# Kernel tuning notes

Measured on AMD Instinct MI355X. Metric: run time of the kernel, lower is better.

Reference implementation:

```python
import jax, jax.numpy as jnp
import numpy as np
from jax import lax

D_MODEL = 1024
D_STATE = 16
D_CONV = 4
EXPAND = 2
D_INNER = EXPAND * D_MODEL  # 2048
DT_RANK = -(-D_MODEL // 16)  # ceil = 64
BATCH = 2
T = 1024


def setup_inputs() -> dict:
    key = jax.random.key(0)
    ks = jax.random.split(key, 9)
    s = 0.02
    x = jax.random.normal(ks[0], (BATCH, T, D_MODEL), dtype=jnp.float32)
    W_in = jax.random.normal(ks[1], (D_MODEL, 2 * D_INNER), dtype=jnp.float32) * s
    conv_w = jax.random.normal(ks[2], (D_INNER, D_CONV), dtype=jnp.float32) * 0.2
    conv_b = jax.random.normal(ks[3], (D_INNER,), dtype=jnp.float32) * 0.02
    W_xproj = jax.random.normal(ks[4], (D_INNER, DT_RANK + 2 * D_STATE), dtype=jnp.float32) * s
    W_dt = jax.random.normal(ks[5], (DT_RANK, D_INNER), dtype=jnp.float32) * s
    b_dt = jax.random.normal(ks[6], (D_INNER,), dtype=jnp.float32) * 0.02
    A_log = jnp.broadcast_to(jnp.log(jnp.arange(1, D_STATE + 1, dtype=jnp.float32)), (D_INNER, D_STATE)).copy()
    D_param = jnp.ones((D_INNER,), dtype=jnp.float32)
    W_out = jax.random.normal(ks[7], (D_INNER, D_MODEL), dtype=jnp.float32) * s
    return {"x": x, "W_in": W_in, "conv_w": conv_w, "conv_b": conv_b,
            "W_xproj": W_xproj, "W_dt": W_dt, "b_dt": b_dt,
            "A_log": A_log, "D_param": D_param, "W_out": W_out}


def _silu(u):
    return u * jax.nn.sigmoid(u)


def _forward(x, W_in, conv_w, conv_b, W_xproj, W_dt, b_dt, A_log, D_param, W_out):
    B, Tlen, _ = x.shape
    # in_proj and split into x-branch and gate z
    xz = x @ W_in                                   # (B,T,2*d_inner)
    x_b, z = jnp.split(xz, 2, axis=-1)              # each (B,T,d_inner)
    # causal depthwise conv1d: y[t] = sum_k w[:,k] * x[t-d_conv+1+k]
    xpad = jnp.pad(x_b, ((0, 0), (D_CONV - 1, 0), (0, 0)))
    xc = conv_b
    for k in range(D_CONV):
        xc = xc + xpad[:, k:k + Tlen, :] * conv_w[:, k]
    xc = _silu(xc)                                  # (B,T,d_inner)
    # SSM parameter projections
    proj = xc @ W_xproj                             # (B,T,dt_rank+2*d_state)
    delta_raw = proj[..., :DT_RANK]
    B_in = proj[..., DT_RANK:DT_RANK + D_STATE]     # (B,T,d_state)
    C_in = proj[..., DT_RANK + D_STATE:]            # (B,T,d_state)
    delta = jax.nn.softplus(delta_raw @ W_dt + b_dt)  # (B,T,d_inner)
    A = -jnp.exp(A_log)                             # (d_inner,d_state)
    A_bar = jnp.exp(delta[..., None] * A)           # (B,T,d_inner,d_state)
    Bx = delta[..., None] * B_in[:, :, None, :] * xc[..., None]  # (B,T,d_inner,d_state)

    def step(h, ins):
        a_t, bx_t, c_t, xc_t = ins
        h = a_t * h + bx_t                          # (B,d_inner,d_state)
        y_t = jnp.einsum('bds,bs->bd', h, c_t) + D_param * xc_t
        return h, y_t

    h0 = jnp.zeros((B, D_INNER, D_STATE), dtype=x.dtype)
    ins = (jnp.swapaxes(A_bar, 0, 1), jnp.swapaxes(Bx, 0, 1),
           jnp.swapaxes(C_in, 0, 1), jnp.swapaxes(xc, 0, 1))
    _, ys = lax.scan(step, h0, ins)                 # ys: (T,B,d_inner)
    y = jnp.swapaxes(ys, 0, 1) * _silu(z)           # gated
    return y @ W_out                                # (B,T,d_model)


def reference(x, W_in, conv_w, conv_b, W_xproj, W_dt, b_dt, A_log, D_param, W_out):
    return _forward(x, W_in, conv_w, conv_b, W_xproj, W_dt, b_dt, A_log, D_param, W_out)
```

## Files before the change

kernel.cpp:

```cpp
#include <hip/hip_runtime.h>
#include <math.h>

#define BATCH   2
#define TLEN    1024
#define DMODEL  1024
#define DINNER  2048
#define DSTATE  16
#define DTRANK  64
#define NPROJ   (DTRANK + 2*DSTATE)
#define CH      32
#define NCH     (TLEN / CH)

typedef __attribute__((ext_vector_type(8))) short short8;
typedef __attribute__((ext_vector_type(4))) float f32x4;

__device__ __forceinline__ float siluf(float u) {
    return u / (1.0f + __expf(-u));
}
__device__ __forceinline__ float softplusf(float x) {
    return (x > 20.0f) ? x : log1pf(__expf(x));
}
__device__ __forceinline__ unsigned short f2bf(float f) {
    union { float f; unsigned u; } v; v.f = f;
    unsigned r = v.u + 0x7FFF + ((v.u >> 16) & 1);
    return (unsigned short)(r >> 16);
}
__device__ __forceinline__ float bf2f(unsigned short u) {
    union { unsigned u; float f; } v; v.u = (unsigned)u << 16;
    return v.f;
}

#define GLOAD_LDS16(g, l) \
  __builtin_amdgcn_global_load_lds( \
     (const __attribute__((address_space(1))) unsigned int*)(g), \
     (__attribute__((address_space(3))) unsigned int*)(l), 16, 0, 0)

template<int NFRAG, int OUTBF, int EPI>
__global__ __launch_bounds__(256)
void gemm_bf16(const unsigned short* __restrict__ A, int lda,
               const unsigned short* __restrict__ BT, int ldb,
               void* __restrict__ Cv, int ldc, int kchunk,
               const float* __restrict__ bias, size_t zstride)
{
    constexpr int BN = NFRAG * 32;
    __shared__ unsigned short As[128 * 32];
    __shared__ unsigned short Bs[BN * 32];

    const int nwg = gridDim.x * gridDim.y;
    int id = blockIdx.y * gridDim.x + blockIdx.x;
    {
        const int q = nwg >> 3, r = nwg & 7, xcd = id & 7, lid = id >> 3;
        id = (xcd < r ? xcd * (q + 1) : r * (q + 1) + (xcd - r) * q) + lid;
    }
    const int bx = id % gridDim.x, by = id / gridDim.x;

    const int tid  = threadIdx.x;
    const int wid  = tid >> 6;
    const int lane = tid & 63;
    const int brow = by * 128;
    const int bcol = bx * BN;
    const int kbeg = blockIdx.z * kchunk;
    const int wr = (wid >> 1) * 64;
    const int wc = (wid & 1) * (NFRAG * 16);
    const int lrow = lane & 15;
    const int lk   = (lane >> 4) * 8;

    f32x4 acc[4][NFRAG] = {};

    for (int k0 = kbeg; k0 < kbeg + kchunk; k0 += 32) {
        #pragma unroll
        for (int it = 0; it < 2; ++it) {
            const int c = it * 256 + tid;
            const unsigned short* g = A + (size_t)(brow + (c >> 2)) * lda + k0 + (c & 3) * 8;
            GLOAD_LDS16(g, As + (size_t)(it * 256 + wid * 64) * 8);
        }
        constexpr int BCH = BN * 4;
        #pragma unroll
        for (int it = 0; it < (BCH + 255) / 256; ++it) {
            const int c = it * 256 + tid;
            if (BCH % 256 == 0 || c < BCH) {
                const unsigned short* g = BT + (size_t)(bcol + (c >> 2)) * ldb + k0 + (c & 3) * 8;
                GLOAD_LDS16(g, Bs + (size_t)(it * 256 + wid * 64) * 8);
            }
        }
        __syncthreads();

        short8 af[4], bfr[NFRAG];
        #pragma unroll
        for (int m = 0; m < 4; ++m)
            af[m] = *(const short8*)(As + (size_t)(wr + m * 16 + lrow) * 32 + lk);
        #pragma unroll
        for (int n = 0; n < NFRAG; ++n)
            bfr[n] = *(const short8*)(Bs + (size_t)(wc + n * 16 + lrow) * 32 + lk);

        #pragma unroll
        for (int m = 0; m < 4; ++m)
            #pragma unroll
            for (int n = 0; n < NFRAG; ++n)
                acc[m][n] = __builtin_amdgcn_mfma_f32_16x16x32_bf16(af[m], bfr[n], acc[m][n], 0, 0, 0);
        __syncthreads();
    }

    const size_t zoff = (size_t)blockIdx.z * zstride;
    const int crow = (lane >> 4) * 4;
    #pragma unroll
    for (int m = 0; m < 4; ++m)
        #pragma unroll
        for (int n = 0; n < NFRAG; ++n) {
            const int gc = bcol + wc + n * 16 + lrow;
            const size_t coff = zoff + (size_t)(brow + wr + m * 16 + crow) * ldc + gc;
            #pragma unroll
            for (int r = 0; r < 4; ++r) {
                float v = acc[m][n][r];
                if (EPI == 1) v = softplusf(v + bias[gc]);
                if (OUTBF)
                    ((unsigned short*)Cv)[coff + (size_t)r * ldc] = f2bf(v);
                else
                    ((float*)Cv)[coff + (size_t)r * ldc] = v;
            }
        }
}

__device__ __forceinline__ void tile_transpose(float (*tile)[33],
        const float* __restrict__ in, unsigned short* __restrict__ out,
        int R, int C, int bx, int by, int tx, int ty)
{
    const int c0 = bx * 32, r0 = by * 32;
    #pragma unroll
    for (int j = 0; j < 32; j += 8)
        tile[ty + j][tx] = in[(size_t)(r0 + ty + j) * C + c0 + tx];
    __syncthreads();
    #pragma unroll
    for (int j = 0; j < 32; j += 8)
        out[(size_t)(c0 + ty + j) * R + r0 + tx] = f2bf(tile[tx][ty + j]);
}

__global__ __launch_bounds__(256)
void prep(const float* __restrict__ x, const float* __restrict__ W_in,
          const float* __restrict__ W_xproj, const float* __restrict__ W_dt,
          const float* __restrict__ W_out,
          unsigned short* __restrict__ x_bf, unsigned short* __restrict__ wt_in,
          unsigned short* __restrict__ wxp_t, unsigned short* __restrict__ wdt_t,
          unsigned short* __restrict__ wt_out)
{
    __shared__ float tile[32][33];
    const int blk = blockIdx.x;
    const int tx = threadIdx.x & 31, ty = threadIdx.x >> 5;
    if (blk < 2048) {
        const int i = blk * 256 + threadIdx.x;
        float4 v = ((const float4*)x)[i];
        union { unsigned short u[4]; uint2 v2; } o;
        o.u[0] = f2bf(v.x); o.u[1] = f2bf(v.y); o.u[2] = f2bf(v.z); o.u[3] = f2bf(v.w);
        ((uint2*)x_bf)[i] = o.v2;
    } else if (blk < 6144) {
        const int lb = blk - 2048;
        tile_transpose(tile, W_in, wt_in, DMODEL, 2*DINNER, lb % 128, lb / 128, tx, ty);
    } else if (blk < 6336) {
        const int lb = blk - 6144;
        tile_transpose(tile, W_xproj, wxp_t, DINNER, NPROJ, lb % 3, lb / 3, tx, ty);
    } else if (blk < 6464) {
        const int lb = blk - 6336;
        tile_transpose(tile, W_dt, wdt_t, DTRANK, DINNER, lb % 64, lb / 64, tx, ty);
    } else {
        const int lb = blk - 6464;
        tile_transpose(tile, W_out, wt_out, DINNER, DMODEL, lb % 32, lb / 32, tx, ty);
    }
}

__global__ __launch_bounds__(256)
void reduce8_dual(const float* __restrict__ in, float* __restrict__ out,
                  unsigned short* __restrict__ draw, int n, size_t zstride)
{
    const int i = blockIdx.x * 256 + threadIdx.x;
    if (i >= n) return;
    float s = 0.f;
    #pragma unroll
    for (int z = 0; z < 8; ++z) s += in[(size_t)z * zstride + i];
    out[i] = s;
    const int row = i / NPROJ;
    const int col = i - row * NPROJ;
    if (col < DTRANK) draw[(size_t)row * DTRANK + col] = f2bf(s);
}

__global__ __launch_bounds__(256)
void conv_silu(const unsigned short* __restrict__ xz, const float* __restrict__ conv_w,
               const float* __restrict__ conv_b, unsigned short* __restrict__ xc)
{
    const int idx = blockIdx.x * 256 + threadIdx.x;
    const int d = idx & (DINNER - 1);
    const int t = (idx >> 11) & (TLEN - 1);
    const int b = idx >> 21;

    const unsigned short* xb = xz + (size_t)b * TLEN * (2*DINNER) + d;
    float s = conv_b[d];
    const float4 w = *(const float4*)(conv_w + d * 4);
    const float wk[4] = {w.x, w.y, w.z, w.w};
    #pragma unroll
    for (int k = 0; k < 4; ++k) {
        const int tt = t + k - 3;
        if (tt >= 0) s = fmaf(bf2f(xb[(size_t)tt * (2*DINNER)]), wk[k], s);
    }
    xc[idx] = f2bf(siluf(s));
}

__global__ __launch_bounds__(256)
void scan1(const unsigned short* __restrict__ delta, const unsigned short* __restrict__ xc,
           const float* __restrict__ proj, const float* __restrict__ A_log,
           unsigned short* __restrict__ hloc, float* __restrict__ sumdel)
{
    const int idx = blockIdx.x * 256 + threadIdx.x;
    const int d = idx & (DINNER - 1);
    const int c = (idx >> 11) & (NCH - 1);
    const int b = idx >> 16;

    float Aa[DSTATE];
    #pragma unroll
    for (int s = 0; s < DSTATE; ++s) Aa[s] = -__expf(A_log[d * DSTATE + s]);

    float h[DSTATE];
    #pragma unroll
    for (int s = 0; s < DSTATE; ++s) h[s] = 0.f;
    float sd = 0.f;

    const int t0 = c * CH;
    const unsigned short* dptr = delta + ((size_t)(b * TLEN + t0)) * DINNER + d;
    const unsigned short* xptr = xc    + ((size_t)(b * TLEN + t0)) * DINNER + d;
    const float* pptr = proj  + ((size_t)(b * TLEN + t0)) * NPROJ;

    for (int t = 0; t < CH; ++t) {
        const float dl = bf2f(dptr[(size_t)t * DINNER]);
        const float xv = bf2f(xptr[(size_t)t * DINNER]);
        const float dx = dl * xv;
        sd += dl;
        #pragma unroll
        for (int s = 0; s < DSTATE; ++s) {
            const float ab = __expf(dl * Aa[s]);
            const float Bv = pptr[t * NPROJ + DTRANK + s];
            h[s] = fmaf(ab, h[s], dx * Bv);
        }
    }
    unsigned u[8];
    #pragma unroll
    for (int i = 0; i < 8; ++i)
        u[i] = (unsigned)f2bf(h[2*i]) | ((unsigned)f2bf(h[2*i+1]) << 16);
    unsigned* hp = (unsigned*)hloc + (((size_t)(b * DINNER + d)) * NCH + c) * 8;
    ((uint4*)hp)[0] = make_uint4(u[0], u[1], u[2], u[3]);
    ((uint4*)hp)[1] = make_uint4(u[4], u[5], u[6], u[7]);
    sumdel[(size_t)(b * DINNER + d) * NCH + c] = sd;
}

__global__ __launch_bounds__(256)
void scan_combine(const unsigned short* __restrict__ hloc, const float* __restrict__ sumdel,
                  const float* __restrict__ A_log, unsigned short* __restrict__ hstart)
{
    __shared__ float hl[32 * 17];
    __shared__ unsigned short hso[32 * 16];
    const int bd  = blockIdx.x;
    const int d   = bd & (DINNER - 1);
    const int tid = threadIdx.x;

    {
        const unsigned v = ((const unsigned*)hloc)[(size_t)bd * 256 + tid];
        const int c = tid >> 3, s0 = (tid & 7) * 2;
        hl[c*17 + s0]     = bf2f((unsigned short)(v & 0xFFFF));
        hl[c*17 + s0 + 1] = bf2f((unsigned short)(v >> 16));
    }
    const int lane32 = tid & 31;
    const int grp    = tid >> 5;
    const float sdv = sumdel[(size_t)bd * NCH + lane32];
    __syncthreads();

    #pragma unroll
    for (int q = 0; q < 2; ++q) {
        const int s = grp * 2 + q;
        const float Aa = -__expf(A_log[d * DSTATE + s]);
        float A  = __expf(Aa * sdv);
        float Bv = hl[lane32*17 + s];
        #pragma unroll
        for (int off = 1; off < 32; off <<= 1) {
            float Ap = __shfl_up(A, off, 32);
            float Bp = __shfl_up(Bv, off, 32);
            if (lane32 >= off) { Bv = fmaf(A, Bp, Bv); A *= Ap; }
        }
        float hsv = __shfl_up(Bv, 1, 32);
        if (lane32 == 0) hsv = 0.f;
        hso[lane32*16 + s] = f2bf(hsv);
    }
    __syncthreads();
    {
        const unsigned v = (unsigned)hso[tid*2] | ((unsigned)hso[tid*2+1] << 16);
        ((unsigned*)hstart)[(size_t)bd * 256 + tid] = v;
    }
}

__global__ __launch_bounds__(256)
void scan2(const unsigned short* __restrict__ delta, const unsigned short* __restrict__ xc,
           const float* __restrict__ proj, const float* __restrict__ A_log,
           const float* __restrict__ D_param, const unsigned short* __restrict__ xz,
           const unsigned short* __restrict__ hstart, unsigned short* __restrict__ y)
{
    const int idx = blockIdx.x * 256 + threadIdx.x;
    const int d = idx & (DINNER - 1);
    const int c = (idx >> 11) & (NCH - 1);
    const int b = idx >> 16;

    float Aa[DSTATE];
    #pragma unroll
    for (int s = 0; s < DSTATE; ++s) Aa[s] = -__expf(A_log[d * DSTATE + s]);

    float h[DSTATE];
    {
        const unsigned* hp = (const unsigned*)hstart + (((size_t)(b * DINNER + d)) * NCH + c) * 8;
        uint4 v0 = ((const uint4*)hp)[0], v1 = ((const uint4*)hp)[1];
        unsigned uu[8] = {v0.x, v0.y, v0.z, v0.w, v1.x, v1.y, v1.z, v1.w};
        #pragma unroll
        for (int i = 0; i < 8; ++i) {
            h[2*i]   = bf2f((unsigned short)(uu[i] & 0xFFFF));
            h[2*i+1] = bf2f((unsigned short)(uu[i] >> 16));
        }
    }

    const float Dp = D_param[d];
    const int t0 = c * CH;
    const unsigned short* dptr = delta + ((size_t)(b * TLEN + t0)) * DINNER + d;
    const unsigned short* xptr = xc    + ((size_t)(b * TLEN + t0)) * DINNER + d;
    const float* pptr = proj  + ((size_t)(b * TLEN + t0)) * NPROJ;
    const unsigned short* zptr = xz + ((size_t)(b * TLEN + t0)) * (2*DINNER) + DINNER + d;
    unsigned short* yptr = y + ((size_t)(b * TLEN + t0)) * DINNER + d;

    for (int t = 0; t < CH; ++t) {
        const float dl = bf2f(dptr[(size_t)t * DINNER]);
        const float xv = bf2f(xptr[(size_t)t * DINNER]);
        const float dx = dl * xv;
        float yt = 0.f;
        #pragma unroll
        for (int s = 0; s < DSTATE; ++s) {
            const float ab = __expf(dl * Aa[s]);
            const float Bv = pptr[t * NPROJ + DTRANK + s];
            h[s] = fmaf(ab, h[s], dx * Bv);
            const float Cv = pptr[t * NPROJ + DTRANK + DSTATE + s];
            yt = fmaf(h[s], Cv, yt);
        }
        yt = fmaf(Dp, xv, yt);
        const float z = bf2f(zptr[(size_t)t * (2*DINNER)]);
        yptr[(size_t)t * DINNER] = f2bf(yt * siluf(z));
    }
}

extern "C" void kernel_launch(void* const* d_in, const int* in_sizes, int n_in,
                              void* d_out, int out_size, void* d_ws, size_t ws_size,
                              hipStream_t stream)
{
    const float* x      = (const float*)d_in[0];
    const float* W_in   = (const float*)d_in[1];
    const float* conv_w = (const float*)d_in[2];
    const float* conv_b = (const float*)d_in[3];
    const float* W_xproj= (const float*)d_in[4];
    const float* W_dt   = (const float*)d_in[5];
    const float* b_dt   = (const float*)d_in[6];
    const float* A_log  = (const float*)d_in[7];
    const float* D_param= (const float*)d_in[8];
    const float* W_out  = (const float*)d_in[9];
    float* out = (float*)d_out;

    float* ws = (float*)d_ws;
    unsigned short* xz_bf    = (unsigned short*)(ws + 0);
    unsigned short* xc_bf    = (unsigned short*)(ws + 4194304);
    float*          proj     = ws + 6291456;
    unsigned short* delta_bf = (unsigned short*)(ws + 6488064);
    unsigned short* hloc     = (unsigned short*)(ws + 8585216);
    float*          sumdel   = ws + 9633792;
    unsigned short* hstart   = (unsigned short*)(ws + 9764864);
    unsigned short* x_bf     = (unsigned short*)(ws + 10813440);
    unsigned short* wt_in    = (unsigned short*)(ws + 11862016);
    unsigned short* wxp_t    = (unsigned short*)(ws + 13959168);
    unsigned short* wdt_t    = (unsigned short*)(ws + 14057472);
    unsigned short* wt_out   = (unsigned short*)(ws + 14123008);
    float*          projp    = ws + 15171584;
    unsigned short* draw_bf  = (unsigned short*)(ws + 16744448);
    unsigned short* yb_bf    = (unsigned short*)(ws + 16809984);

    dim3 blk(256);

    prep<<<8512, blk, 0, stream>>>(x, W_in, W_xproj, W_dt, W_out,
                                   x_bf, wt_in, wxp_t, wdt_t, wt_out);

    gemm_bf16<4,1,0><<<dim3(2*DINNER/128, 2048/128), blk, 0, stream>>>(
        x_bf, DMODEL, wt_in, DMODEL, xz_bf, 2*DINNER, DMODEL, nullptr, 0);

    conv_silu<<<(BATCH*TLEN*DINNER)/256, blk, 0, stream>>>(xz_bf, conv_w, conv_b, xc_bf);

    gemm_bf16<3,0,0><<<dim3(1, 2048/128, 8), blk, 0, stream>>>(
        xc_bf, DINNER, wxp_t, DINNER, projp, NPROJ, DINNER/8, nullptr, 196608);
    reduce8_dual<<<768, blk, 0, stream>>>(projp, proj, draw_bf, 196608, 196608);

    gemm_bf16<4,1,1><<<dim3(2048/128, 2048/128), blk, 0, stream>>>(
        draw_bf, DTRANK, wdt_t, DTRANK, delta_bf, DINNER, DTRANK, b_dt, 0);

    scan1<<<(BATCH*NCH*DINNER)/256, blk, 0, stream>>>(delta_bf, xc_bf, proj, A_log, hloc, sumdel);
    scan_combine<<<BATCH*DINNER, blk, 0, stream>>>(hloc, sumdel, A_log, hstart);
    scan2<<<(BATCH*NCH*DINNER)/256, blk, 0, stream>>>(delta_bf, xc_bf, proj, A_log, D_param, xz_bf, hstart, yb_bf);

    gemm_bf16<2,0,0><<<dim3(DMODEL/64, 2048/128), blk, 0, stream>>>(
        yb_bf, DINNER, wt_out, DINNER, out, DMODEL, DINNER, nullptr, 0);
}
```

Before: 274.3 us.

## Retile GEMMs with configurable M tile, vectorize conv, deepen xproj split-K

The GEMM kernel gets an MFRAG template parameter so row tiles can shrink. The in-proj, dt-proj and out-proj GEMMs now use smaller tiles and launch more workgroups, and the xproj GEMM splits K sixteen ways instead of eight, with a matching 16-way reduce. The conv+SiLU kernel now handles 8 channels per thread using 16-byte vector loads and stores. The aim is better occupancy and coalescing across the 256 CUs. The cost is less data reuse per tile and more partial-sum traffic for the reduction.

```diff
diff --git a/kernel.cpp b/kernel.cpp
--- a/kernel.cpp
+++ b/kernel.cpp
@@ -35,15 +35,16 @@
      (const __attribute__((address_space(1))) unsigned int*)(g), \
      (__attribute__((address_space(3))) unsigned int*)(l), 16, 0, 0)
 
-template<int NFRAG, int OUTBF, int EPI>
+template<int MFRAG, int NFRAG, int OUTBF, int EPI>
 __global__ __launch_bounds__(256)
 void gemm_bf16(const unsigned short* __restrict__ A, int lda,
                const unsigned short* __restrict__ BT, int ldb,
                void* __restrict__ Cv, int ldc, int kchunk,
                const float* __restrict__ bias, size_t zstride)
 {
+    constexpr int BM = MFRAG * 32;
     constexpr int BN = NFRAG * 32;
-    __shared__ unsigned short As[128 * 32];
+    __shared__ unsigned short As[BM * 32];
     __shared__ unsigned short Bs[BN * 32];
 
     const int nwg = gridDim.x * gridDim.y;
@@ -57,22 +58,25 @@
     const int tid  = threadIdx.x;
     const int wid  = tid >> 6;
     const int lane = tid & 63;
-    const int brow = by * 128;
+    const int brow = by * BM;
     const int bcol = bx * BN;
     const int kbeg = blockIdx.z * kchunk;
-    const int wr = (wid >> 1) * 64;
+    const int wr = (wid >> 1) * (MFRAG * 16);
     const int wc = (wid & 1) * (NFRAG * 16);
     const int lrow = lane & 15;
     const int lk   = (lane >> 4) * 8;
 
-    f32x4 acc[4][NFRAG] = {};
+    f32x4 acc[MFRAG][NFRAG] = {};
 
     for (int k0 = kbeg; k0 < kbeg + kchunk; k0 += 32) {
-        #pragma unroll
-        for (int it = 0; it < 2; ++it) {
+        constexpr int ACH = BM * 4;
+        #pragma unroll
+        for (int it = 0; it < (ACH + 255) / 256; ++it) {
             const int c = it * 256 + tid;
-            const unsigned short* g = A + (size_t)(brow + (c >> 2)) * lda + k0 + (c & 3) * 8;
-            GLOAD_LDS16(g, As + (size_t)(it * 256 + wid * 64) * 8);
+            if (ACH % 256 == 0 || c < ACH) {
+                const unsigned short* g = A + (size_t)(brow + (c >> 2)) * lda + k0 + (c & 3) * 8;
+                GLOAD_LDS16(g, As + (size_t)(it * 256 + wid * 64) * 8);
+            }
         }
         constexpr int BCH = BN * 4;
         #pragma unroll
@@ -85,16 +89,16 @@
         }
         __syncthreads();
 
-        short8 af[4], bfr[NFRAG];
-        #pragma unroll
-        for (int m = 0; m < 4; ++m)
+        short8 af[MFRAG], bfr[NFRAG];
+        #pragma unroll
+        for (int m = 0; m < MFRAG; ++m)
             af[m] = *(const short8*)(As + (size_t)(wr + m * 16 + lrow) * 32 + lk);
         #pragma unroll
         for (int n = 0; n < NFRAG; ++n)
             bfr[n] = *(const short8*)(Bs + (size_t)(wc + n * 16 + lrow) * 32 + lk);
 
         #pragma unroll
-        for (int m = 0; m < 4; ++m)
+        for (int m = 0; m < MFRAG; ++m)
             #pragma unroll
             for (int n = 0; n < NFRAG; ++n)
                 acc[m][n] = __builtin_amdgcn_mfma_f32_16x16x32_bf16(af[m], bfr[n], acc[m][n], 0, 0, 0);
@@ -104,7 +108,7 @@
     const size_t zoff = (size_t)blockIdx.z * zstride;
     const int crow = (lane >> 4) * 4;
     #pragma unroll
-    for (int m = 0; m < 4; ++m)
+    for (int m = 0; m < MFRAG; ++m)
         #pragma unroll
         for (int n = 0; n < NFRAG; ++n) {
             const int gc = bcol + wc + n * 16 + lrow;
@@ -168,14 +172,14 @@
 }
 
 __global__ __launch_bounds__(256)
-void reduce8_dual(const float* __restrict__ in, float* __restrict__ out,
-                  unsigned short* __restrict__ draw, int n, size_t zstride)
+void reduce16_dual(const float* __restrict__ in, float* __restrict__ out,
+                   unsigned short* __restrict__ draw, int n, size_t zstride)
 {
     const int i = blockIdx.x * 256 + threadIdx.x;
     if (i >= n) return;
     float s = 0.f;
     #pragma unroll
-    for (int z = 0; z < 8; ++z) s += in[(size_t)z * zstride + i];
+    for (int z = 0; z < 16; ++z) s += in[(size_t)z * zstride + i];
     out[i] = s;
     const int row = i / NPROJ;
     const int col = i - row * NPROJ;
@@ -186,21 +190,43 @@
 void conv_silu(const unsigned short* __restrict__ xz, const float* __restrict__ conv_w,
                const float* __restrict__ conv_b, unsigned short* __restrict__ xc)
 {
-    const int idx = blockIdx.x * 256 + threadIdx.x;
-    const int d = idx & (DINNER - 1);
-    const int t = (idx >> 11) & (TLEN - 1);
-    const int b = idx >> 21;
+    const int i = blockIdx.x * 256 + threadIdx.x;
+    const int e = i * 8;
+    const int d = e & (DINNER - 1);
+    const int t = (e >> 11) & (TLEN - 1);
+    const int b = e >> 21;
+
+    float acc[8];
+    {
+        const float4 b0 = *(const float4*)(conv_b + d);
+        const float4 b1 = *(const float4*)(conv_b + d + 4);
+        acc[0]=b0.x; acc[1]=b0.y; acc[2]=b0.z; acc[3]=b0.w;
+        acc[4]=b1.x; acc[5]=b1.y; acc[6]=b1.z; acc[7]=b1.w;
+    }
+    float4 w4[8];
+    #pragma unroll
+    for (int j = 0; j < 8; ++j) w4[j] = *(const float4*)(conv_w + (d + j) * 4);
 
     const unsigned short* xb = xz + (size_t)b * TLEN * (2*DINNER) + d;
-    float s = conv_b[d];
-    const float4 w = *(const float4*)(conv_w + d * 4);
-    const float wk[4] = {w.x, w.y, w.z, w.w};
     #pragma unroll
     for (int k = 0; k < 4; ++k) {
         const int tt = t + k - 3;
-        if (tt >= 0) s = fmaf(bf2f(xb[(size_t)tt * (2*DINNER)]), wk[k], s);
-    }
-    xc[idx] = f2bf(siluf(s));
+        if (tt >= 0) {
+            const short8 v = *(const short8*)(xb + (size_t)tt * (2*DINNER));
+            const float wk[8] = {w4[0].x, w4[1].x, w4[2].x, w4[3].x,
+                                 w4[4].x, w4[5].x, w4[6].x, w4[7].x};
+            #pragma unroll
+            for (int j = 0; j < 8; ++j) {
+                float wv = (k==0) ? w4[j].x : (k==1) ? w4[j].y : (k==2) ? w4[j].z : w4[j].w;
+                acc[j] = fmaf(bf2f((unsigned short)v[j]), wv, acc[j]);
+            }
+            (void)wk;
+        }
+    }
+    short8 o;
+    #pragma unroll
+    for (int j = 0; j < 8; ++j) o[j] = (short)f2bf(siluf(acc[j]));
+    *(short8*)(xc + (size_t)i * 8) = o;
 }
 
 __global__ __launch_bounds__(256)
@@ -377,30 +403,30 @@
     unsigned short* wdt_t    = (unsigned short*)(ws + 14057472);
     unsigned short* wt_out   = (unsigned short*)(ws + 14123008);
     float*          projp    = ws + 15171584;
-    unsigned short* draw_bf  = (unsigned short*)(ws + 16744448);
-    unsigned short* yb_bf    = (unsigned short*)(ws + 16809984);
+    unsigned short* draw_bf  = (unsigned short*)(ws + 18317312);
+    unsigned short* yb_bf    = (unsigned short*)(ws + 18382848);
 
     dim3 blk(256);
 
     prep<<<8512, blk, 0, stream>>>(x, W_in, W_xproj, W_dt, W_out,
                                    x_bf, wt_in, wxp_t, wdt_t, wt_out);
 
-    gemm_bf16<4,1,0><<<dim3(2*DINNER/128, 2048/128), blk, 0, stream>>>(
+    gemm_bf16<4,2,1,0><<<dim3(4096/64, 2048/128), blk, 0, stream>>>(
         x_bf, DMODEL, wt_in, DMODEL, xz_bf, 2*DINNER, DMODEL, nullptr, 0);
 
-    conv_silu<<<(BATCH*TLEN*DINNER)/256, blk, 0, stream>>>(xz_bf, conv_w, conv_b, xc_bf);
-
-    gemm_bf16<3,0,0><<<dim3(1, 2048/128, 8), blk, 0, stream>>>(
-        xc_bf, DINNER, wxp_t, DINNER, projp, NPROJ, DINNER/8, nullptr, 196608);
-    reduce8_dual<<<768, blk, 0, stream>>>(projp, proj, draw_bf, 196608, 196608);
-
-    gemm_bf16<4,1,1><<<dim3(2048/128, 2048/128), blk, 0, stream>>>(
+    conv_silu<<<(BATCH*TLEN*DINNER/8)/256, blk, 0, stream>>>(xz_bf, conv_w, conv_b, xc_bf);
+
+    gemm_bf16<2,3,0,0><<<dim3(1, 2048/64, 16), blk, 0, stream>>>(
+        xc_bf, DINNER, wxp_t, DINNER, projp, NPROJ, DINNER/16, nullptr, 196608);
+    reduce16_dual<<<768, blk, 0, stream>>>(projp, proj, draw_bf, 196608, 196608);
+
+    gemm_bf16<4,2,1,1><<<dim3(2048/64, 2048/128), blk, 0, stream>>>(
         draw_bf, DTRANK, wdt_t, DTRANK, delta_bf, DINNER, DTRANK, b_dt, 0);
 
     scan1<<<(BATCH*NCH*DINNER)/256, blk, 0, stream>>>(delta_bf, xc_bf, proj, A_log, hloc, sumdel);
     scan_combine<<<BATCH*DINNER, blk, 0, stream>>>(hloc, sumdel, A_log, hstart);
     scan2<<<(BATCH*NCH*DINNER)/256, blk, 0, stream>>>(delta_bf, xc_bf, proj, A_log, D_param, xz_bf, hstart, yb_bf);
 
-    gemm_bf16<2,0,0><<<dim3(DMODEL/64, 2048/128), blk, 0, stream>>>(
+    gemm_bf16<2,2,0,0><<<dim3(1024/64, 2048/64), blk, 0, stream>>>(
         yb_bf, DINNER, wt_out, DINNER, out, DMODEL, DINNER, nullptr, 0);
 }
```

Measured after the change: 260.2 us. 5.1% less time.
